# Kernel tuning notes

Measured on AMD Instinct MI355X. Metric: run time of the kernel, lower is better.

Reference implementation:

```python
import jax, jax.numpy as jnp
import numpy as np

B, L, DN, DE, DD, H = 8, 256, 256, 128, 64, 8
DK, DEH, DDH = DN // H, DE // H, DD // H
NEG = 0.2


def _lin(x, w, b):
    return x @ w.T + b


def _lrelu(x):
    return jnp.where(x >= 0, x, NEG * x)


def setup_inputs() -> dict:
    key = jax.random.key(0)
    ks = jax.random.split(key, 24)
    def w(k, shape):
        return jax.random.normal(k, shape, jnp.float32) * 0.02
    din = 2 * DK + DEH + 2 * DDH  # 96
    return {
        "node": jax.random.normal(ks[0], (B, L, DN), jnp.float32),
        "edge": jax.random.normal(ks[1], (B, L, L, DE), jnp.float32),
        "diff": jax.random.normal(ks[2], (B, L, DD), jnp.float32),
        "Wn_w": w(ks[3], (DN, DN)), "Wn_b": w(ks[4], (DN,)),
        "Wh_w": w(ks[5], (DK, DK)), "Wh_b": w(ks[6], (DK,)),
        "We_w": w(ks[7], (DE, DE)), "We_b": w(ks[8], (DE,)),
        "Wn2_w": w(ks[9], (DN, DN)), "Wn2_b": w(ks[10], (DN,)),
        "We2_w": w(ks[11], (DE, DE)), "We2_b": w(ks[12], (DE,)),
        "Wd_w": w(ks[13], (DD, DD)), "Wd_b": w(ks[14], (DD,)),
        "Wd2_w": w(ks[15], (DD, DD)), "Wd2_b": w(ks[16], (DD,)),
        "attn_w": w(ks[17], (1, din)),
        "edge_lin_w": w(ks[18], (DEH, din)), "edge_lin_b": w(ks[19], (DEH,)),
        "outn_w": w(ks[20], (DN, DN)), "outn_b": w(ks[21], (DN,)),
        "oute_w": w(ks[22], (DE, DE)), "oute_b": w(ks[23], (DE,)),
    }


def reference(node, edge, diff, Wn_w, Wn_b, Wh_w, Wh_b, We_w, We_b,
              Wn2_w, Wn2_b, We2_w, We2_b, Wd_w, Wd_b, Wd2_w, Wd2_b,
              attn_w, edge_lin_w, edge_lin_b, outn_w, outn_b, oute_w, oute_b):
    Bn, Ln, _ = node.shape
    eye = jnp.eye(Ln, dtype=bool)

    # ---- stage 1: node update (per-head concat-based GAT attention) ----
    hp = _lin(node, Wn_w, Wn_b).reshape(Bn, Ln, H, DK)        # Wn
    ep = _lin(edge, We_w, We_b).reshape(Bn, Ln, Ln, H, DEH)   # We
    dp = _lin(diff, Wd_w, Wd_b).reshape(Bn, Ln, H, DDH)       # Wd
    # attn_linear(cat[hi, hj, eij, di, dj]) decomposes additively (no bias)
    a = attn_w[0]
    a_hi, a_hj = a[:DK], a[DK:2 * DK]
    a_e = a[2 * DK:2 * DK + DEH]
    a_di = a[2 * DK + DEH:2 * DK + DEH + DDH]
    a_dj = a[2 * DK + DEH + DDH:]
    s_i = jnp.einsum('blhd,d->blh', hp, a_hi) + jnp.einsum('blhd,d->blh', dp, a_di)
    s_j = jnp.einsum('blhd,d->blh', hp, a_hj) + jnp.einsum('blhd,d->blh', dp, a_dj)
    s_e = jnp.einsum('bijhd,d->bijh', ep, a_e)
    scores = _lrelu(s_i[:, :, None, :] + s_j[:, None, :, :] + s_e)   # [B,L,L,H]
    scores = jnp.where(eye[None, :, :, None], jnp.finfo(scores.dtype).min, scores)
    probs = jax.nn.softmax(scores, axis=2)  # softmax over j != i
    whh = _lin(hp, Wh_w, Wh_b)              # Wh shared across heads, [B,L,H,DK]
    agg = jnp.einsum('bijh,bjhd->bihd', probs, whh)
    new_node = _lin((hp + _lrelu(agg)).reshape(Bn, Ln, DN), outn_w, outn_b)

    # ---- stage 2: edge update ----
    hp2 = _lin(new_node, Wn2_w, Wn2_b).reshape(Bn, Ln, H, DK)
    ep2 = _lin(edge, We2_w, We2_b).reshape(Bn, Ln, Ln, H, DEH)
    dp2 = _lin(diff, Wd2_w, Wd2_b).reshape(Bn, Ln, H, DDH)
    # edge_linear(cat[eij, hi, hj, di, dj]) decomposed into blocks
    W_e = edge_lin_w[:, :DEH]
    W_hi = edge_lin_w[:, DEH:DEH + DK]
    W_hj = edge_lin_w[:, DEH + DK:DEH + 2 * DK]
    W_di = edge_lin_w[:, DEH + 2 * DK:DEH + 2 * DK + DDH]
    W_dj = edge_lin_w[:, DEH + 2 * DK + DDH:]
    t_i = jnp.einsum('blhd,ed->blhe', hp2, W_hi) + jnp.einsum('blhd,ed->blhe', dp2, W_di)
    t_j = jnp.einsum('blhd,ed->blhe', hp2, W_hj) + jnp.einsum('blhd,ed->blhe', dp2, W_dj)
    t_e = jnp.einsum('bijhd,ed->bijhe', ep2, W_e)
    new_e = t_e + t_i[:, :, None] + t_j[:, None] + edge_lin_b   # [B,L,L,H,DEH]
    new_e = jnp.where(eye[None, :, :, None, None], 0.0, new_e)  # diagonal stays 0
    new_edge = _lin(new_e.reshape(Bn, Ln, Ln, DE), oute_w, oute_b)
    return (new_node, new_edge)
```

## Files before the change

### kernel.cpp

```cpp
#include <hip/hip_runtime.h>
#include <cstdint>
#include <cstddef>

#define NBATCH 8
#define LSEQ   256
#define NODE_CNT 2048

#define OFF_HP      0u
#define OFF_DP      524288u
#define OFF_SI      655360u
#define OFF_SJ      671744u
#define OFF_WHH     688128u
#define OFF_U       1212416u
#define OFF_V       1474560u
#define OFF_CE      1737728u
#define OFF_CT      1737760u
#define OFF_K0      1754144u
#define OFF_D       1754272u
#define OFF_CONSTE  1770656u
#define OFF_GT      1770784u
#define OFF_WN1T    1771840u
#define OFF_WN2T    1837376u
#define OFF_WNT     1902912u
#define OFF_OUTET   1968448u
#define OFF_WD1T    1984832u
#define OFF_WD2T    1988928u
#define OFF_WHT     1993024u

#define GT_PITCH 132
#define SC_PITCH 264

__device__ __forceinline__ float lrelu(float x){ return x >= 0.f ? x : 0.2f*x; }

__global__ void k_pre_a(const float* __restrict__ We_w, const float* __restrict__ We_b,
                        const float* __restrict__ attn_w,
                        const float* __restrict__ edge_lin_w, const float* __restrict__ edge_lin_b,
                        const float* __restrict__ We2_w, const float* __restrict__ We2_b,
                        float* __restrict__ ws) {
    int tid = threadIdx.x;
    const float* a_e = attn_w + 64;
    for (int idx = tid; idx < 128*8; idx += 256) {
        int k = idx >> 3, h = idx & 7;
        float s = 0.f;
        for (int e = 0; e < 16; ++e) s += a_e[e] * We_w[(h*16+e)*128 + k];
        ws[OFF_GT + h*GT_PITCH + k] = s;
    }
    if (tid < 8) {
        float s = 0.f;
        for (int e = 0; e < 16; ++e) s += a_e[e] * We_b[tid*16+e];
        ws[OFF_CE + tid] = s;
    }
    for (int idx = tid; idx < 128*128; idx += 256) {
        int m = idx >> 7, k = idx & 127;
        int h = m >> 4, eo = m & 15;
        float s = 0.f;
        for (int ei = 0; ei < 16; ++ei) s += edge_lin_w[eo*96 + ei] * We2_w[(h*16+ei)*128 + k];
        ws[OFF_D + m*128 + k] = s;
    }
    if (tid < 128) {
        int h = tid >> 4, eo = tid & 15;
        float s = edge_lin_b[eo];
        for (int ei = 0; ei < 16; ++ei) s += edge_lin_w[eo*96+ei] * We2_b[h*16+ei];
        ws[OFF_CONSTE + tid] = s;
    }
}

__global__ void k_pre_b(const float* __restrict__ oute_w, const float* __restrict__ oute_b,
                        float* __restrict__ ws) {
    int idx = blockIdx.x*256 + threadIdx.x;
    int k = idx >> 7, n2 = idx & 127;
    const float* D = ws + OFF_D;
    float s = 0.f;
    for (int m = 0; m < 128; ++m) s += oute_w[n2*128+m] * D[m*128+k];
    ws[OFF_CT + k*128 + n2] = s;
    if (blockIdx.x == 0 && threadIdx.x < 128) {
        int n = threadIdx.x;
        float t = oute_b[n];
        const float* ce = ws + OFF_CONSTE;
        for (int m = 0; m < 128; ++m) t += oute_w[n*128+m]*ce[m];
        ws[OFF_K0 + n] = t;
    }
}

__global__ void k_transpose(const float* __restrict__ Wn_w, const float* __restrict__ Wn2_w,
                            const float* __restrict__ outn_w, const float* __restrict__ oute_w,
                            const float* __restrict__ Wd_w, const float* __restrict__ Wd2_w,
                            const float* __restrict__ Wh_w, float* __restrict__ ws) {
    int bx = blockIdx.x, tid = threadIdx.x;
    const float* src; float* dst; int ln, base;
    if      (bx < 256) { src = Wn_w;   dst = ws + OFF_WN1T;  ln = 8; base = bx; }
    else if (bx < 512) { src = Wn2_w;  dst = ws + OFF_WN2T;  ln = 8; base = bx - 256; }
    else if (bx < 768) { src = outn_w; dst = ws + OFF_WNT;   ln = 8; base = bx - 512; }
    else if (bx < 832) { src = oute_w; dst = ws + OFF_OUTET; ln = 7; base = bx - 768; }
    else if (bx < 848) { src = Wd_w;   dst = ws + OFF_WD1T;  ln = 6; base = bx - 832; }
    else if (bx < 864) { src = Wd2_w;  dst = ws + OFF_WD2T;  ln = 6; base = bx - 848; }
    else               { src = Wh_w;   dst = ws + OFF_WHT;   ln = 5; base = bx - 864; }
    int idx = base*256 + tid;
    int N = 1 << ln;
    int k = idx >> ln, n = idx & (N-1);
    dst[idx] = src[n*N + k];
}

__global__ __launch_bounds__(256)
void k_node1(const float* __restrict__ node, const float* __restrict__ diff,
             const float* __restrict__ Wn_b, const float* __restrict__ Wd_b,
             const float* __restrict__ Wh_b, const float* __restrict__ attn_w,
             float* __restrict__ ws) {
    __shared__ float nrow[8][256];
    __shared__ float drow[8][64];
    __shared__ float hprow[8][256];
    __shared__ float dprow[8][64];
    int tid = threadIdx.x;
    int n0 = blockIdx.x * 8;
    #pragma unroll
    for (int t = 0; t < 8; ++t) nrow[t][tid] = node[(size_t)(n0+t)*256 + tid];
    if (tid < 64) {
        #pragma unroll
        for (int t = 0; t < 8; ++t) drow[t][tid] = diff[(n0+t)*64 + tid];
    }
    __syncthreads();
    {
        const float* WT = ws + OFF_WN1T;
        float acc[8] = {0,0,0,0,0,0,0,0};
        for (int k = 0; k < 256; k += 4) {
            float w0 = WT[(k  )*256+tid], w1 = WT[(k+1)*256+tid];
            float w2 = WT[(k+2)*256+tid], w3 = WT[(k+3)*256+tid];
            #pragma unroll
            for (int t = 0; t < 8; ++t) {
                float4 n4 = *(const float4*)&nrow[t][k];
                acc[t] += n4.x*w0 + n4.y*w1 + n4.z*w2 + n4.w*w3;
            }
        }
        float b = Wn_b[tid];
        #pragma unroll
        for (int t = 0; t < 8; ++t) {
            float v = acc[t] + b;
            ws[OFF_HP + (size_t)(n0+t)*256 + tid] = v;
            hprow[t][tid] = v;
        }
    }
    if (tid < 64) {
        const float* WT = ws + OFF_WD1T;
        float acc[8] = {0,0,0,0,0,0,0,0};
        for (int k = 0; k < 64; k += 4) {
            float w0 = WT[(k  )*64+tid], w1 = WT[(k+1)*64+tid];
            float w2 = WT[(k+2)*64+tid], w3 = WT[(k+3)*64+tid];
            #pragma unroll
            for (int t = 0; t < 8; ++t) {
                float4 d4 = *(const float4*)&drow[t][k];
                acc[t] += d4.x*w0 + d4.y*w1 + d4.z*w2 + d4.w*w3;
            }
        }
        float b = Wd_b[tid];
        #pragma unroll
        for (int t = 0; t < 8; ++t) {
            float v = acc[t] + b;
            ws[OFF_DP + (n0+t)*64 + tid] = v;
            dprow[t][tid] = v;
        }
    }
    __syncthreads();
    {
        int h = tid >> 5, d = tid & 31;
        const float* WT = ws + OFF_WHT;
        float acc[8] = {0,0,0,0,0,0,0,0};
        for (int k = 0; k < 32; k += 4) {
            float w0 = WT[(k  )*32+d], w1 = WT[(k+1)*32+d];
            float w2 = WT[(k+2)*32+d], w3 = WT[(k+3)*32+d];
            #pragma unroll
            for (int t = 0; t < 8; ++t) {
                float4 h4 = *(const float4*)&hprow[t][h*32+k];
                acc[t] += h4.x*w0 + h4.y*w1 + h4.z*w2 + h4.w*w3;
            }
        }
        float b = Wh_b[d];
        #pragma unroll
        for (int t = 0; t < 8; ++t) ws[OFF_WHH + (size_t)(n0+t)*256 + tid] = acc[t] + b;
    }
    if (tid < 16) {
        int h = tid & 7; bool isj = tid >= 8;
        const float* ah = attn_w + (isj ? 32 : 0);
        const float* ad = attn_w + (isj ? 88 : 80);
        for (int t = 0; t < 8; ++t) {
            float s = 0.f;
            for (int k = 0; k < 32; ++k) s += hprow[t][h*32+k]*ah[k];
            for (int k = 0; k < 8;  ++k) s += dprow[t][h*8+k]*ad[k];
            ws[(isj ? OFF_SJ : OFF_SI) + (n0+t)*8 + h] = s;
        }
    }
}

__global__ __launch_bounds__(256, 4)
void k_phase1(const float* __restrict__ edge, float* __restrict__ ws,
              const float* __restrict__ outn_b, float* __restrict__ out_node) {
    __shared__ float sc[8*SC_PITCH];
    __shared__ float GsT[8*GT_PITCH];
    __shared__ float sjs[2048];
    __shared__ float cEs[8], sirow[8], hinv[8];
    __shared__ float hprow[256];
    __shared__ float arow[256];
    int tid = threadIdx.x;
    int bl = blockIdx.x;
    int i = bl & 255;
    int base_b = bl & ~255;
    for (int idx = tid; idx < 8*GT_PITCH; idx += 256) GsT[idx] = ws[OFF_GT + idx];
    #pragma unroll
    for (int q = 0; q < 8; ++q) sjs[q*256+tid] = ws[OFF_SJ + base_b*8 + q*256 + tid];
    if (tid < 8) { cEs[tid] = ws[OFF_CE + tid]; sirow[tid] = ws[OFF_SI + bl*8 + tid]; }
    hprow[tid] = ws[OFF_HP + (size_t)bl*256 + tid];
    __syncthreads();

    {
        int jj = tid >> 3, h = tid & 7;
        const float* erow = edge + (size_t)bl*256*128;
        float acc[8] = {0,0,0,0,0,0,0,0};
        for (int kt = 0; kt < 128; kt += 16) {
            float g[16];
            #pragma unroll
            for (int q = 0; q < 4; ++q)
                *(float4*)&g[q*4] = *(const float4*)&GsT[h*GT_PITCH + kt + q*4];
            #pragma unroll
            for (int t = 0; t < 8; ++t) {
                const float* ev = erow + (size_t)(t*32+jj)*128 + kt;
                float4 e0 = ((const float4*)ev)[0];
                float4 e1 = ((const float4*)ev)[1];
                float4 e2 = ((const float4*)ev)[2];
                float4 e3 = ((const float4*)ev)[3];
                acc[t] += e0.x*g[0] + e0.y*g[1] + e0.z*g[2] + e0.w*g[3]
                        + e1.x*g[4] + e1.y*g[5] + e1.z*g[6] + e1.w*g[7]
                        + e2.x*g[8] + e2.y*g[9] + e2.z*g[10]+ e2.w*g[11]
                        + e3.x*g[12]+ e3.y*g[13]+ e3.z*g[14]+ e3.w*g[15];
            }
        }
        float ce = cEs[h], si = sirow[h];
        #pragma unroll
        for (int t = 0; t < 8; ++t) {
            int j = t*32 + jj;
            float s = acc[t] + ce + si + sjs[j*8+h];
            s = lrelu(s);
            if (j == i) s = -3.4028235e38f;
            sc[h*SC_PITCH + j] = s;
        }
    }
    __syncthreads();
    {
        int g = tid >> 5, lane = tid & 31;
        float m = -3.4028235e38f;
        #pragma unroll
        for (int t = 0; t < 8; ++t) m = fmaxf(m, sc[g*SC_PITCH + lane + 32*t]);
        for (int off = 16; off >= 1; off >>= 1) m = fmaxf(m, __shfl_xor(m, off, 32));
        float ssum = 0.f;
        #pragma unroll
        for (int t = 0; t < 8; ++t) {
            int j = lane + 32*t;
            float e = __expf(sc[g*SC_PITCH + j] - m);
            sc[g*SC_PITCH + j] = e;
            ssum += e;
        }
        for (int off = 16; off >= 1; off >>= 1) ssum += __shfl_xor(ssum, off, 32);
        if (lane == 0) hinv[g] = 1.f/ssum;
    }
    __syncthreads();
    {
        int hh = tid >> 5;
        const float* whh = ws + OFF_WHH + (size_t)base_b*256;
        const float* scr = sc + hh*SC_PITCH;
        float a0=0.f, a1=0.f, a2=0.f, a3=0.f;
        #pragma unroll 2
        for (int j = 0; j < 256; j += 4) {
            a0 += scr[j  ]*whh[(size_t)(j  )*256 + tid];
            a1 += scr[j+1]*whh[(size_t)(j+1)*256 + tid];
            a2 += scr[j+2]*whh[(size_t)(j+2)*256 + tid];
            a3 += scr[j+3]*whh[(size_t)(j+3)*256 + tid];
        }
        float acc = ((a0+a1)+(a2+a3)) * hinv[hh];
        arow[tid] = hprow[tid] + lrelu(acc);
    }
    __syncthreads();
    {
        const float* WT = ws + OFF_WNT;
        float o0=0.f, o1=0.f, o2=0.f, o3=0.f;
        #pragma unroll 2
        for (int m = 0; m < 256; m += 4) {
            o0 += arow[m  ]*WT[(m  )*256 + tid];
            o1 += arow[m+1]*WT[(m+1)*256 + tid];
            o2 += arow[m+2]*WT[(m+2)*256 + tid];
            o3 += arow[m+3]*WT[(m+3)*256 + tid];
        }
        out_node[(size_t)bl*256 + tid] = outn_b[tid] + ((o0+o1)+(o2+o3));
    }
}

__global__ __launch_bounds__(256)
void k_node2(const float* __restrict__ out_node, const float* __restrict__ diff,
             const float* __restrict__ Wn2_b, const float* __restrict__ Wd2_b,
             const float* __restrict__ edge_lin_w, float* __restrict__ ws) {
    __shared__ float nrow[8][256];
    __shared__ float drow[8][64];
    __shared__ float hp2[8][256];
    __shared__ float dp2[8][64];
    __shared__ float tij[2][8][128];
    int tid = threadIdx.x;
    int n0 = blockIdx.x * 8;
    #pragma unroll
    for (int t = 0; t < 8; ++t) nrow[t][tid] = out_node[(size_t)(n0+t)*256 + tid];
    if (tid < 64) {
        #pragma unroll
        for (int t = 0; t < 8; ++t) drow[t][tid] = diff[(n0+t)*64 + tid];
    }
    __syncthreads();
    {
        const float* WT = ws + OFF_WN2T;
        float acc[8] = {0,0,0,0,0,0,0,0};
        for (int k = 0; k < 256; k += 4) {
            float w0 = WT[(k  )*256+tid], w1 = WT[(k+1)*256+tid];
            float w2 = WT[(k+2)*256+tid], w3 = WT[(k+3)*256+tid];
            #pragma unroll
            for (int t = 0; t < 8; ++t) {
                float4 n4 = *(const float4*)&nrow[t][k];
                acc[t] += n4.x*w0 + n4.y*w1 + n4.z*w2 + n4.w*w3;
            }
        }
        float b = Wn2_b[tid];
        #pragma unroll
        for (int t = 0; t < 8; ++t) hp2[t][tid] = acc[t] + b;
    }
    if (tid < 64) {
        const float* WT = ws + OFF_WD2T;
        float acc[8] = {0,0,0,0,0,0,0,0};
        for (int k = 0; k < 64; k += 4) {
            float w0 = WT[(k  )*64+tid], w1 = WT[(k+1)*64+tid];
            float w2 = WT[(k+2)*64+tid], w3 = WT[(k+3)*64+tid];
            #pragma unroll
            for (int t = 0; t < 8; ++t) {
                float4 d4 = *(const float4*)&drow[t][k];
                acc[t] += d4.x*w0 + d4.y*w1 + d4.z*w2 + d4.w*w3;
            }
        }
        float b = Wd2_b[tid];
        #pragma unroll
        for (int t = 0; t < 8; ++t) dp2[t][tid] = acc[t] + b;
    }
    __syncthreads();
    for (int q = 0; q < 8; ++q) {
        int idx = q*256 + tid;
        int s = idx >> 10; int r = idx & 1023; int t = r >> 7; int m = r & 127;
        int h = m >> 4, eo = m & 15;
        const float* wh = edge_lin_w + eo*96 + (s ? 48 : 16);
        const float* wd = edge_lin_w + eo*96 + (s ? 88 : 80);
        float v = 0.f;
        for (int d = 0; d < 32; ++d) v += hp2[t][h*32+d]*wh[d];
        for (int d = 0; d < 8;  ++d) v += dp2[t][h*8+d]*wd[d];
        tij[s][t][m] = v;
    }
    __syncthreads();
    for (int q = 0; q < 8; ++q) {
        int idx = q*256 + tid;
        int s = idx >> 10; int r = idx & 1023; int t = r >> 7; int n2 = r & 127;
        const float* OT = ws + OFF_OUTET;
        const float* tv = tij[s][t];
        float a0 = 0.f, a1 = 0.f;
        #pragma unroll 2
        for (int m = 0; m < 128; m += 2) {
            a0 += tv[m  ]*OT[(m  )*128 + n2];
            a1 += tv[m+1]*OT[(m+1)*128 + n2];
        }
        ws[(s ? OFF_V : OFF_U) + (n0+t)*128 + n2] = a0 + a1;
    }
}

#define KKSTEP(F, KOFF) { \
    float4 b0 = *(const float4*)&CTs[(kq+KOFF)*128 + n2b]; \
    float4 b1 = *(const float4*)&CTs[(kq+KOFF)*128 + n2b + 4]; \
    _Pragma("unroll") \
    for (int p = 0; p < 8; ++p) { float av = a4[p].F; \
        acc[p][0] += av*b0.x; acc[p][1] += av*b0.y; acc[p][2] += av*b0.z; acc[p][3] += av*b0.w; \
        acc[p][4] += av*b1.x; acc[p][5] += av*b1.y; acc[p][6] += av*b1.z; acc[p][7] += av*b1.w; } }

__global__ __launch_bounds__(256, 2)
void k_edge2(const float* __restrict__ edge, const float* __restrict__ oute_b,
             const float* __restrict__ ws, float* __restrict__ out_edge) {
    __shared__ float CTs[128*128];
    int tid = threadIdx.x;
    int bx = blockIdx.x;
    int bl = bx >> 1, jh = bx & 1;
    int i = bl & 255, base_b = bl & ~255;
    for (int idx = tid; idx < 16384; idx += 256) CTs[idx] = ws[OFF_CT + idx];
    __syncthreads();
    int tj = tid >> 4, tn = tid & 15;
    int n2b = tn*8;
    const float* erow = edge + (size_t)bl*256*128 + (size_t)(jh*128 + tj*8)*128;
    float acc[8][8];
    #pragma unroll
    for (int p = 0; p < 8; ++p)
        #pragma unroll
        for (int q = 0; q < 8; ++q) acc[p][q] = 0.f;

    for (int kq = 0; kq < 128; kq += 4) {
        float4 a4[8];
        #pragma unroll
        for (int p = 0; p < 8; ++p) a4[p] = *(const float4*)(erow + (size_t)p*128 + kq);
        KKSTEP(x, 0) KKSTEP(y, 1) KKSTEP(z, 2) KKSTEP(w, 3)
    }

    const float* uP = ws + OFF_U + (size_t)bl*128 + n2b;
    float4 u0 = *(const float4*)uP, u1 = *(const float4*)(uP+4);
    const float* cP = ws + OFF_K0 + n2b;
    float4 c0 = *(const float4*)cP, c1 = *(const float4*)(cP+4);
    float4 ob0 = *(const float4*)(oute_b + n2b), ob1 = *(const float4*)(oute_b + n2b + 4);
    #pragma unroll
    for (int p = 0; p < 8; ++p) {
        int j = jh*128 + tj*8 + p;
        const float* vP = ws + OFF_V + (size_t)(base_b + j)*128 + n2b;
        float4 v0 = *(const float4*)vP, v1 = *(const float4*)(vP+4);
        float4 o0, o1;
        o0.x = acc[p][0]+u0.x+v0.x+c0.x; o0.y = acc[p][1]+u0.y+v0.y+c0.y;
        o0.z = acc[p][2]+u0.z+v0.z+c0.z; o0.w = acc[p][3]+u0.w+v0.w+c0.w;
        o1.x = acc[p][4]+u1.x+v1.x+c1.x; o1.y = acc[p][5]+u1.y+v1.y+c1.y;
        o1.z = acc[p][6]+u1.z+v1.z+c1.z; o1.w = acc[p][7]+u1.w+v1.w+c1.w;
        if (j == i) { o0 = ob0; o1 = ob1; }
        float* oP = out_edge + ((size_t)bl*256 + j)*128 + n2b;
        *(float4*)oP = o0; *(float4*)(oP+4) = o1;
    }
}

extern "C" void kernel_launch(void* const* d_in, const int* in_sizes, int n_in,
                              void* d_out, int out_size, void* d_ws, size_t ws_size,
                              hipStream_t stream) {
    const float* node   = (const float*)d_in[0];
    const float* edge   = (const float*)d_in[1];
    const float* diff   = (const float*)d_in[2];
    const float* Wn_w   = (const float*)d_in[3];
    const float* Wn_b   = (const float*)d_in[4];
    const float* Wh_w   = (const float*)d_in[5];
    const float* Wh_b   = (const float*)d_in[6];
    const float* We_w   = (const float*)d_in[7];
    const float* We_b   = (const float*)d_in[8];
    const float* Wn2_w  = (const float*)d_in[9];
    const float* Wn2_b  = (const float*)d_in[10];
    const float* We2_w  = (const float*)d_in[11];
    const float* We2_b  = (const float*)d_in[12];
    const float* Wd_w   = (const float*)d_in[13];
    const float* Wd_b   = (const float*)d_in[14];
    const float* Wd2_w  = (const float*)d_in[15];
    const float* Wd2_b  = (const float*)d_in[16];
    const float* attn_w = (const float*)d_in[17];
    const float* elw    = (const float*)d_in[18];
    const float* elb    = (const float*)d_in[19];
    const float* outn_w = (const float*)d_in[20];
    const float* outn_b = (const float*)d_in[21];
    const float* oute_w = (const float*)d_in[22];
    const float* oute_b = (const float*)d_in[23];
    float* ws = (float*)d_ws;
    float* out_node = (float*)d_out;
    float* out_edge = out_node + (size_t)NODE_CNT*256;

    k_pre_a<<<1, 256, 0, stream>>>(We_w, We_b, attn_w, elw, elb, We2_w, We2_b, ws);
    k_pre_b<<<64, 256, 0, stream>>>(oute_w, oute_b, ws);
    k_transpose<<<868, 256, 0, stream>>>(Wn_w, Wn2_w, outn_w, oute_w, Wd_w, Wd2_w, Wh_w, ws);
    k_node1<<<256, 256, 0, stream>>>(node, diff, Wn_b, Wd_b, Wh_b, attn_w, ws);
    k_phase1<<<NODE_CNT, 256, 0, stream>>>(edge, ws, outn_b, out_node);
    k_node2<<<256, 256, 0, stream>>>(out_node, diff, Wn2_b, Wd2_b, elw, ws);
    k_edge2<<<NODE_CNT*2, 256, 0, stream>>>(edge, oute_b, ws, out_edge);
}
```

Baseline: 917.0 us.

## Use split-bf16 MFMA for the edge output GEMM

Rewrites k_edge2 to compute the edge-to-output projection with bf16 MFMA instructions. Each fp32 operand is split into high and low bf16 halves and three products are summed to keep accuracy close to fp32. A new prep kernel pre-splits the folded weight matrix into high and low bf16 arrays, which are stored in swizzled shared memory. Blocks now cover a whole 256-row i slice with 512 threads. k_pre_b reads the transposed oute_w, so the launch order is changed to run the transpose first. The intent is to replace the scalar FMA GEMM that dominates runtime with matrix-core work, at the cost of in-kernel conversion and scattered scalar stores.

```diff
diff --git a/kernel.cpp b/kernel.cpp
--- a/kernel.cpp
+++ b/kernel.cpp
@@ -17,6 +17,8 @@
 #define OFF_CT      1737760u
 #define OFF_K0      1754144u
 #define OFF_D       1754272u
+#define OFF_CTH     1754272u
+#define OFF_CTL     1762464u
 #define OFF_CONSTE  1770656u
 #define OFF_GT      1770784u
 #define OFF_WN1T    1771840u
@@ -30,57 +32,12 @@
 #define GT_PITCH 132
 #define SC_PITCH 264
 
+typedef __attribute__((ext_vector_type(8))) __bf16 bf16x8;
+typedef __attribute__((ext_vector_type(8))) unsigned short ushort8;
+typedef __attribute__((ext_vector_type(4))) float f32x4;
+typedef __attribute__((ext_vector_type(4))) unsigned int u32x4;
+
 __device__ __forceinline__ float lrelu(float x){ return x >= 0.f ? x : 0.2f*x; }
-
-__global__ void k_pre_a(const float* __restrict__ We_w, const float* __restrict__ We_b,
-                        const float* __restrict__ attn_w,
-                        const float* __restrict__ edge_lin_w, const float* __restrict__ edge_lin_b,
-                        const float* __restrict__ We2_w, const float* __restrict__ We2_b,
-                        float* __restrict__ ws) {
-    int tid = threadIdx.x;
-    const float* a_e = attn_w + 64;
-    for (int idx = tid; idx < 128*8; idx += 256) {
-        int k = idx >> 3, h = idx & 7;
-        float s = 0.f;
-        for (int e = 0; e < 16; ++e) s += a_e[e] * We_w[(h*16+e)*128 + k];
-        ws[OFF_GT + h*GT_PITCH + k] = s;
-    }
-    if (tid < 8) {
-        float s = 0.f;
-        for (int e = 0; e < 16; ++e) s += a_e[e] * We_b[tid*16+e];
-        ws[OFF_CE + tid] = s;
-    }
-    for (int idx = tid; idx < 128*128; idx += 256) {
-        int m = idx >> 7, k = idx & 127;
-        int h = m >> 4, eo = m & 15;
-        float s = 0.f;
-        for (int ei = 0; ei < 16; ++ei) s += edge_lin_w[eo*96 + ei] * We2_w[(h*16+ei)*128 + k];
-        ws[OFF_D + m*128 + k] = s;
-    }
-    if (tid < 128) {
-        int h = tid >> 4, eo = tid & 15;
-        float s = edge_lin_b[eo];
-        for (int ei = 0; ei < 16; ++ei) s += edge_lin_w[eo*96+ei] * We2_b[h*16+ei];
-        ws[OFF_CONSTE + tid] = s;
-    }
-}
-
-__global__ void k_pre_b(const float* __restrict__ oute_w, const float* __restrict__ oute_b,
-                        float* __restrict__ ws) {
-    int idx = blockIdx.x*256 + threadIdx.x;
-    int k = idx >> 7, n2 = idx & 127;
-    const float* D = ws + OFF_D;
-    float s = 0.f;
-    for (int m = 0; m < 128; ++m) s += oute_w[n2*128+m] * D[m*128+k];
-    ws[OFF_CT + k*128 + n2] = s;
-    if (blockIdx.x == 0 && threadIdx.x < 128) {
-        int n = threadIdx.x;
-        float t = oute_b[n];
-        const float* ce = ws + OFF_CONSTE;
-        for (int m = 0; m < 128; ++m) t += oute_w[n*128+m]*ce[m];
-        ws[OFF_K0 + n] = t;
-    }
-}
 
 __global__ void k_transpose(const float* __restrict__ Wn_w, const float* __restrict__ Wn2_w,
                             const float* __restrict__ outn_w, const float* __restrict__ oute_w,
@@ -99,6 +56,71 @@
     int N = 1 << ln;
     int k = idx >> ln, n = idx & (N-1);
     dst[idx] = src[n*N + k];
+}
+
+__global__ void k_pre_a(const float* __restrict__ We_w, const float* __restrict__ We_b,
+                        const float* __restrict__ attn_w,
+                        const float* __restrict__ edge_lin_w, const float* __restrict__ edge_lin_b,
+                        const float* __restrict__ We2_w, const float* __restrict__ We2_b,
+                        float* __restrict__ ws) {
+    int tid = threadIdx.x;
+    const float* a_e = attn_w + 64;
+    for (int idx = tid; idx < 128*8; idx += 256) {
+        int h = idx >> 7, k = idx & 127;
+        float s = 0.f;
+        for (int e = 0; e < 16; ++e) s += a_e[e] * We_w[(h*16+e)*128 + k];
+        ws[OFF_GT + h*GT_PITCH + k] = s;
+    }
+    if (tid < 8) {
+        float s = 0.f;
+        for (int e = 0; e < 16; ++e) s += a_e[e] * We_b[tid*16+e];
+        ws[OFF_CE + tid] = s;
+    }
+    for (int idx = tid; idx < 128*128; idx += 256) {
+        int m = idx >> 7, k = idx & 127;
+        int h = m >> 4, eo = m & 15;
+        float s = 0.f;
+        for (int ei = 0; ei < 16; ++ei) s += edge_lin_w[eo*96 + ei] * We2_w[(h*16+ei)*128 + k];
+        ws[OFF_D + m*128 + k] = s;
+    }
+    if (tid < 128) {
+        int h = tid >> 4, eo = tid & 15;
+        float s = edge_lin_b[eo];
+        for (int ei = 0; ei < 16; ++ei) s += edge_lin_w[eo*96+ei] * We2_b[h*16+ei];
+        ws[OFF_CONSTE + tid] = s;
+    }
+}
+
+__global__ void k_pre_b(const float* __restrict__ oute_b, float* __restrict__ ws) {
+    int idx = blockIdx.x*256 + threadIdx.x;
+    int k = idx >> 7, n2 = idx & 127;
+    const float* D  = ws + OFF_D;
+    const float* OT = ws + OFF_OUTET;
+    float s = 0.f;
+    for (int m = 0; m < 128; ++m) s += OT[m*128+n2] * D[m*128+k];
+    ws[OFF_CT + k*128 + n2] = s;
+    if (blockIdx.x == 0 && threadIdx.x < 128) {
+        int n = threadIdx.x;
+        float t = oute_b[n];
+        const float* ce = ws + OFF_CONSTE;
+        for (int m = 0; m < 128; ++m) t += OT[m*128+n]*ce[m];
+        ws[OFF_K0 + n] = t;
+    }
+}
+
+__global__ void k_pre_c(float* __restrict__ ws) {
+    int idx = blockIdx.x*256 + threadIdx.x;
+    int k = idx >> 7, n = idx & 127;
+    float s = ws[OFF_CT + k*128 + n];
+    unsigned int u = __builtin_bit_cast(unsigned int, s);
+    unsigned int h = u >> 16;
+    float fh = __builtin_bit_cast(float, h << 16);
+    float rem = s - fh;
+    unsigned short lo = (unsigned short)(__builtin_bit_cast(unsigned int, rem) >> 16);
+    unsigned short* cth = (unsigned short*)(ws + OFF_CTH);
+    unsigned short* ctl = (unsigned short*)(ws + OFF_CTL);
+    cth[n*128 + k] = (unsigned short)h;
+    ctl[n*128 + k] = lo;
 }
 
 __global__ __launch_bounds__(256)
@@ -369,58 +391,97 @@
     }
 }
 
-#define KKSTEP(F, KOFF) { \
-    float4 b0 = *(const float4*)&CTs[(kq+KOFF)*128 + n2b]; \
-    float4 b1 = *(const float4*)&CTs[(kq+KOFF)*128 + n2b + 4]; \
-    _Pragma("unroll") \
-    for (int p = 0; p < 8; ++p) { float av = a4[p].F; \
-        acc[p][0] += av*b0.x; acc[p][1] += av*b0.y; acc[p][2] += av*b0.z; acc[p][3] += av*b0.w; \
-        acc[p][4] += av*b1.x; acc[p][5] += av*b1.y; acc[p][6] += av*b1.z; acc[p][7] += av*b1.w; } }
-
-__global__ __launch_bounds__(256, 2)
+__global__ __launch_bounds__(512, 4)
 void k_edge2(const float* __restrict__ edge, const float* __restrict__ oute_b,
              const float* __restrict__ ws, float* __restrict__ out_edge) {
-    __shared__ float CTs[128*128];
+    __shared__ __align__(16) char smem[65536];
     int tid = threadIdx.x;
-    int bx = blockIdx.x;
-    int bl = bx >> 1, jh = bx & 1;
+    int bl = blockIdx.x;
     int i = bl & 255, base_b = bl & ~255;
-    for (int idx = tid; idx < 16384; idx += 256) CTs[idx] = ws[OFF_CT + idx];
-    __syncthreads();
-    int tj = tid >> 4, tn = tid & 15;
-    int n2b = tn*8;
-    const float* erow = edge + (size_t)bl*256*128 + (size_t)(jh*128 + tj*8)*128;
-    float acc[8][8];
+
+    {
+        const u32x4* srcH = (const u32x4*)(ws + OFF_CTH);
+        const u32x4* srcL = (const u32x4*)(ws + OFF_CTL);
+        for (int c = tid; c < 2048; c += 512) {
+            int n = c >> 4;
+            int off = ((n << 8) + ((c & 15) << 4)) ^ ((n & 7) << 4);
+            *(u32x4*)(smem + off)         = srcH[c];
+            *(u32x4*)(smem + 32768 + off) = srcL[c];
+        }
+    }
+    __syncthreads();
+
+    int w = tid >> 6, l = tid & 63;
+    int col = l & 15, kq = l >> 4;
+    int r0 = w * 32;
+    const float* eb = edge + (size_t)bl * 32768;
+    int swz = (col & 7) << 4;
+
+    f32x4 acc[2][8] = {};
+
     #pragma unroll
-    for (int p = 0; p < 8; ++p)
-        #pragma unroll
-        for (int q = 0; q < 8; ++q) acc[p][q] = 0.f;
-
-    for (int kq = 0; kq < 128; kq += 4) {
-        float4 a4[8];
-        #pragma unroll
-        for (int p = 0; p < 8; ++p) a4[p] = *(const float4*)(erow + (size_t)p*128 + kq);
-        KKSTEP(x, 0) KKSTEP(y, 1) KKSTEP(z, 2) KKSTEP(w, 3)
-    }
-
-    const float* uP = ws + OFF_U + (size_t)bl*128 + n2b;
-    float4 u0 = *(const float4*)uP, u1 = *(const float4*)(uP+4);
-    const float* cP = ws + OFF_K0 + n2b;
-    float4 c0 = *(const float4*)cP, c1 = *(const float4*)(cP+4);
-    float4 ob0 = *(const float4*)(oute_b + n2b), ob1 = *(const float4*)(oute_b + n2b + 4);
+    for (int ks = 0; ks < 4; ++ks) {
+        bf16x8 ah[2], al[2];
+        #pragma unroll
+        for (int mt = 0; mt < 2; ++mt) {
+            const float* ap = eb + (size_t)(r0 + mt*16 + col) * 128 + ks*32 + kq*8;
+            float4 e0 = *(const float4*)ap;
+            float4 e1 = *(const float4*)(ap + 4);
+            float ev[8] = {e0.x, e0.y, e0.z, e0.w, e1.x, e1.y, e1.z, e1.w};
+            ushort8 hs, ls;
+            #pragma unroll
+            for (int q = 0; q < 8; ++q) {
+                unsigned int u = __builtin_bit_cast(unsigned int, ev[q]);
+                unsigned int h = u >> 16;
+                float fh = __builtin_bit_cast(float, h << 16);
+                float rem = ev[q] - fh;
+                hs[q] = (unsigned short)h;
+                ls[q] = (unsigned short)(__builtin_bit_cast(unsigned int, rem) >> 16);
+            }
+            ah[mt] = __builtin_bit_cast(bf16x8, hs);
+            al[mt] = __builtin_bit_cast(bf16x8, ls);
+        }
+        bf16x8 bh[8], blo[8];
+        #pragma unroll
+        for (int nt = 0; nt < 8; ++nt) {
+            int n = nt*16 + col;
+            int off = ((n << 8) + (ks << 6) + (kq << 4)) ^ swz;
+            bh[nt]  = __builtin_bit_cast(bf16x8, *(const u32x4*)(smem + off));
+            blo[nt] = __builtin_bit_cast(bf16x8, *(const u32x4*)(smem + 32768 + off));
+        }
+        #pragma unroll
+        for (int nt = 0; nt < 8; ++nt) {
+            #pragma unroll
+            for (int mt = 0; mt < 2; ++mt) {
+                acc[mt][nt] = __builtin_amdgcn_mfma_f32_16x16x32_bf16(ah[mt], bh[nt],  acc[mt][nt], 0, 0, 0);
+                acc[mt][nt] = __builtin_amdgcn_mfma_f32_16x16x32_bf16(al[mt], bh[nt],  acc[mt][nt], 0, 0, 0);
+                acc[mt][nt] = __builtin_amdgcn_mfma_f32_16x16x32_bf16(ah[mt], blo[nt], acc[mt][nt], 0, 0, 0);
+            }
+        }
+    }
+
+    float uk[8], ob[8];
     #pragma unroll
-    for (int p = 0; p < 8; ++p) {
-        int j = jh*128 + tj*8 + p;
-        const float* vP = ws + OFF_V + (size_t)(base_b + j)*128 + n2b;
-        float4 v0 = *(const float4*)vP, v1 = *(const float4*)(vP+4);
-        float4 o0, o1;
-        o0.x = acc[p][0]+u0.x+v0.x+c0.x; o0.y = acc[p][1]+u0.y+v0.y+c0.y;
-        o0.z = acc[p][2]+u0.z+v0.z+c0.z; o0.w = acc[p][3]+u0.w+v0.w+c0.w;
-        o1.x = acc[p][4]+u1.x+v1.x+c1.x; o1.y = acc[p][5]+u1.y+v1.y+c1.y;
-        o1.z = acc[p][6]+u1.z+v1.z+c1.z; o1.w = acc[p][7]+u1.w+v1.w+c1.w;
-        if (j == i) { o0 = ob0; o1 = ob1; }
-        float* oP = out_edge + ((size_t)bl*256 + j)*128 + n2b;
-        *(float4*)oP = o0; *(float4*)(oP+4) = o1;
+    for (int nt = 0; nt < 8; ++nt) {
+        int n = nt*16 + col;
+        uk[nt] = ws[OFF_U + (size_t)bl*128 + n] + ws[OFF_K0 + n];
+        ob[nt] = oute_b[n];
+    }
+    #pragma unroll
+    for (int mt = 0; mt < 2; ++mt) {
+        #pragma unroll
+        for (int q = 0; q < 4; ++q) {
+            int jrow = r0 + mt*16 + kq*4 + q;
+            const float* vrow = ws + OFF_V + (size_t)(base_b + jrow)*128;
+            float* orow = out_edge + ((size_t)bl*256 + jrow)*128;
+            bool diag = (jrow == i);
+            #pragma unroll
+            for (int nt = 0; nt < 8; ++nt) {
+                int n = nt*16 + col;
+                float val = acc[mt][nt][q] + uk[nt] + vrow[n];
+                orow[n] = diag ? ob[nt] : val;
+            }
+        }
     }
 }
 
@@ -455,11 +516,12 @@
     float* out_node = (float*)d_out;
     float* out_edge = out_node + (size_t)NODE_CNT*256;
 
+    k_transpose<<<868, 256, 0, stream>>>(Wn_w, Wn2_w, outn_w, oute_w, Wd_w, Wd2_w, Wh_w, ws);
     k_pre_a<<<1, 256, 0, stream>>>(We_w, We_b, attn_w, elw, elb, We2_w, We2_b, ws);
-    k_pre_b<<<64, 256, 0, stream>>>(oute_w, oute_b, ws);
-    k_transpose<<<868, 256, 0, stream>>>(Wn_w, Wn2_w, outn_w, oute_w, Wd_w, Wd2_w, Wh_w, ws);
+    k_pre_b<<<64, 256, 0, stream>>>(oute_b, ws);
+    k_pre_c<<<64, 256, 0, stream>>>(ws);
     k_node1<<<256, 256, 0, stream>>>(node, diff, Wn_b, Wd_b, Wh_b, attn_w, ws);
     k_phase1<<<NODE_CNT, 256, 0, stream>>>(edge, ws, outn_b, out_node);
     k_node2<<<256, 256, 0, stream>>>(out_node, diff, Wn2_b, Wd2_b, elw, ws);
-    k_edge2<<<NODE_CNT*2, 256, 0, stream>>>(edge, oute_b, ws, out_edge);
-}
+    k_edge2<<<NODE_CNT, 512, 0, stream>>>(edge, oute_b, ws, out_edge);
+}
```

Result: faster. 790.2 us (-13.8%).
